# Kernel optimization log

Measured on AMD Instinct MI355X. Metric: run time of the kernel, lower is better.

Reference implementation:

```python
import jax, jax.numpy as jnp
import numpy as np

B, S, D, H = 8, 1024, 1024, 16
DH = D // H


def setup_inputs() -> dict:
    key = jax.random.key(0)
    ks = jax.random.split(key, 8)
    en = jax.random.normal(ks[0], (B, S, D), dtype=jnp.float32)
    fr = jax.random.normal(ks[1], (B, S, D), dtype=jnp.float32)
    l_en = jax.random.randint(ks[2], (B,), 1, S + 1)
    l_fr = jax.random.randint(ks[3], (B,), 1, S + 1)
    # nn.Linear-style params (weight stored [out, in])
    lim_q = 1.0 / np.sqrt(D)
    W_Q_w = jax.random.uniform(ks[4], (D, D), minval=-lim_q, maxval=lim_q, dtype=jnp.float32)
    W_Q_b = jax.random.uniform(ks[5], (D,), minval=-lim_q, maxval=lim_q, dtype=jnp.float32)
    W_KV_w = jax.random.uniform(ks[6], (2 * D, D), minval=-lim_q, maxval=lim_q, dtype=jnp.float32)
    W_KV_b = jax.random.uniform(ks[7], (2 * D,), minval=-lim_q, maxval=lim_q, dtype=jnp.float32)
    return {"en": en, "fr": fr, "l_en": l_en, "l_fr": l_fr,
            "W_Q_w": W_Q_w, "W_Q_b": W_Q_b, "W_KV_w": W_KV_w, "W_KV_b": W_KV_b}


def reference(en, fr, l_en, l_fr, W_Q_w, W_Q_b, W_KV_w, W_KV_b):
    # q from decoder (fr), k/v from encoder (en)
    q = (fr @ W_Q_w.T + W_Q_b).reshape(B, S, H, DH).transpose(0, 2, 1, 3)  # [B,H,S,DH]
    kv = (en @ W_KV_w.T + W_KV_b).reshape(B, S, 2, H, DH).transpose(2, 0, 3, 1, 4)
    k, v = kv[0], kv[1]  # [B,H,S,DH]

    # NOTE: original scales by sqrt(embedding_dim), not sqrt(head_dim)
    attn = jnp.einsum('bhqd,bhkd->bhqk', q, k) / jnp.sqrt(jnp.float32(D))

    pos = jnp.arange(S)
    mask_en = (pos[None, :] < l_en[:, None])  # [B,S] key mask
    mask_fr = (pos[None, :] < l_fr[:, None])  # [B,S] query mask
    mask = (mask_fr[:, :, None] & mask_en[:, None, :])[:, None, :, :]  # [B,1,Sq,Sk]

    attn = jnp.where(mask, attn, -jnp.inf)
    attn = jax.nn.softmax(attn, axis=-1)
    attn = jnp.nan_to_num(attn)  # fully-masked rows -> 0 (matches torch nan_to_num)

    out = jnp.einsum('bhqk,bhkd->bhqd', attn, v)  # [B,H,S,DH]
    return out.transpose(0, 2, 1, 3).reshape(B, S, D)
```

## Files before the change

### kernel.cpp

```cpp
#include <hip/hip_runtime.h>
#include <hip/hip_bf16.h>
#include <stdint.h>

typedef __bf16 bf16_t;
typedef bf16_t bf16x8 __attribute__((ext_vector_type(8)));
typedef float f32x4 __attribute__((ext_vector_type(4)));
typedef unsigned short ushortx8 __attribute__((ext_vector_type(8)));

__device__ __forceinline__ uint16_t f2bf(float f) {
  uint32_t u = __float_as_uint(f);
  uint32_t r = u + 0x7FFFu + ((u >> 16) & 1u);
  return (uint16_t)(r >> 16);
}

__device__ __forceinline__ int read_len(const int* __restrict__ p, int b) {
  bool is64 = (p[1] == 0) | (p[3] == 0) | (p[5] == 0) | (p[7] == 0);
  return is64 ? p[2 * b] : p[b];
}

#define GLDS16(gp, lp)                                                   \
  __builtin_amdgcn_global_load_lds(                                      \
      (const __attribute__((address_space(1))) uint32_t*)(gp),           \
      (__attribute__((address_space(3))) uint32_t*)(lp), 16, 0, 0)

__global__ void cvt4_kernel(const float* __restrict__ s0, uint16_t* __restrict__ d0, int n0,
                            const float* __restrict__ s1, uint16_t* __restrict__ d1, int n1,
                            const float* __restrict__ s2, uint16_t* __restrict__ d2, int n2,
                            const float* __restrict__ s3, uint16_t* __restrict__ d3, int n3,
                            const int* __restrict__ msk2, const int* __restrict__ msk3) {
  int e = (blockIdx.x * blockDim.x + threadIdx.x) * 4;
  const float* s;
  uint16_t* d;
  const int* msk = nullptr;
  if (e < n0) { s = s0 + e; d = d0 + e; }
  else if ((e -= n0) < n1) { s = s1 + e; d = d1 + e; }
  else if ((e -= n1) < n2) { s = s2 + e; d = d2 + e; msk = msk2; }
  else if ((e -= n2) < n3) { s = s3 + e; d = d3 + e; msk = msk3; }
  else return;
  if (msk) {
    int row = (e >> 10) & 1023, b = e >> 20;
    int need = (read_len(msk, b) + 127) & ~127;
    if (row >= need) return;
  }
  const float4 v = *reinterpret_cast<const float4*>(s);
  ushort4 o;
  o.x = f2bf(v.x); o.y = f2bf(v.y); o.z = f2bf(v.z); o.w = f2bf(v.w);
  *reinterpret_cast<ushort4*>(d) = o;
}

template <bool ABF16>
__global__ __launch_bounds__(256) void gemm_fused(
    const float* __restrict__ frF, const float* __restrict__ enF,
    const uint16_t* __restrict__ frB, const uint16_t* __restrict__ enB,
    const uint16_t* __restrict__ wq, const uint16_t* __restrict__ wkv,
    const float* __restrict__ bq, const float* __restrict__ bkv,
    const int* __restrict__ l_en_p, const int* __restrict__ l_fr_p,
    uint16_t* __restrict__ Qb,
    uint16_t* __restrict__ Kb,
    uint16_t* __restrict__ Vb) {
  __shared__ __attribute__((aligned(16))) uint16_t As[2][128 * 64];
  __shared__ __attribute__((aligned(16))) uint16_t Bs[2][128 * 64];
  const int t = threadIdx.x;
  const int lane = t & 63;
  const int w = t >> 6;
  const int wm = w >> 1, wn = w & 1;
  const int l15 = lane & 15, lg = lane >> 4;

  const int orig = blockIdx.x;
  const int xcd = orig & 7;
  const int slot = orig >> 3;
  const bool isQ = slot < 64;
  int b, bn;
  if (isQ) { b = slot >> 3; bn = (slot & 7) * 128; }
  else { int s2 = slot - 64; b = s2 >> 4; bn = (s2 & 15) * 128; }
  const int i = (xcd - b) & 7;
  const int bm = b * 1024 + i * 128;

  const int need = isQ ? read_len(l_fr_p, b) : read_len(l_en_p, b);
  if (i * 128 >= need) return;

  const uint16_t* Bw = isQ ? wq : wkv;
  const float* bias = isQ ? bq : bkv;
  const float scale = isQ ? 0.03125f : 1.0f;
  const uint16_t* Ab = isQ ? frB : enB;
  const float* Af = isQ ? frF : enF;

  f32x4 acc[4][4];
#pragma unroll
  for (int ii = 0; ii < 4; ++ii)
#pragma unroll
    for (int j = 0; j < 4; ++j) acc[ii][j] = (f32x4){0.f, 0.f, 0.f, 0.f};

  float4 ar0[4], ar1[4];

  auto stageB = [&](int buf, int kt) {
#pragma unroll
    for (int ii = 0; ii < 4; ++ii) {
      int g = t + 256 * ii;
      int L = g ^ ((g >> 3) & 7);
      int row = L >> 3, k8 = L & 7;
      GLDS16(Bw + (size_t)(bn + row) * 1024 + kt + k8 * 8, &Bs[buf][g * 8]);
    }
  };
  auto stageA_bf = [&](int buf, int kt) {
#pragma unroll
    for (int ii = 0; ii < 4; ++ii) {
      int g = t + 256 * ii;
      int L = g ^ ((g >> 3) & 7);
      int row = L >> 3, k8 = L & 7;
      GLDS16(Ab + (size_t)(bm + row) * 1024 + kt + k8 * 8, &As[buf][g * 8]);
    }
  };
  auto loadA_f32 = [&](int kt) {
#pragma unroll
    for (int ii = 0; ii < 4; ++ii) {
      int L = t + 256 * ii;
      int row = L >> 3, k8 = L & 7;
      const float* src = Af + (size_t)(bm + row) * 1024 + kt + k8 * 8;
      ar0[ii] = *reinterpret_cast<const float4*>(src);
      ar1[ii] = *reinterpret_cast<const float4*>(src + 4);
    }
  };
  auto writeA = [&](int buf) {
#pragma unroll
    for (int ii = 0; ii < 4; ++ii) {
      int L = t + 256 * ii;
      int row = L >> 3, k8 = L & 7;
      ushortx8 o;
      o[0] = f2bf(ar0[ii].x); o[1] = f2bf(ar0[ii].y);
      o[2] = f2bf(ar0[ii].z); o[3] = f2bf(ar0[ii].w);
      o[4] = f2bf(ar1[ii].x); o[5] = f2bf(ar1[ii].y);
      o[6] = f2bf(ar1[ii].z); o[7] = f2bf(ar1[ii].w);
      int byte = (row * 128 + k8 * 16) ^ ((row & 7) << 4);
      *reinterpret_cast<ushortx8*>(reinterpret_cast<char*>(As[buf]) + byte) = o;
    }
  };
  auto compute = [&](int buf) {
#pragma unroll
    for (int ks = 0; ks < 2; ++ks) {
      const int kb = ks * 64 + lg * 16;
      bf16x8 af[4], bf[4];
#pragma unroll
      for (int mf = 0; mf < 4; ++mf) {
        int row = wm * 64 + mf * 16 + l15;
        int byte = (row * 128 + kb) ^ ((row & 7) << 4);
        af[mf] = *reinterpret_cast<const bf16x8*>(
            reinterpret_cast<const char*>(As[buf]) + byte);
      }
#pragma unroll
      for (int nf = 0; nf < 4; ++nf) {
        int row = wn * 64 + nf * 16 + l15;
        int byte = (row * 128 + kb) ^ ((row & 7) << 4);
        bf[nf] = *reinterpret_cast<const bf16x8*>(
            reinterpret_cast<const char*>(Bs[buf]) + byte);
      }
#pragma unroll
      for (int mf = 0; mf < 4; ++mf)
#pragma unroll
        for (int nf = 0; nf < 4; ++nf)
          acc[mf][nf] = __builtin_amdgcn_mfma_f32_16x16x32_bf16(
              af[mf], bf[nf], acc[mf][nf], 0, 0, 0);
    }
  };

  if (ABF16) {
    stageB(0, 0);
    stageA_bf(0, 0);
  } else {
    loadA_f32(0);
    stageB(0, 0);
    writeA(0);
  }
  __syncthreads();

#pragma unroll 2
  for (int tt = 0; tt < 16; ++tt) {
    const int cur = tt & 1;
    const int ktn = (tt + 1) * 64;
    if (ABF16) {
      if (tt < 15) { stageB(cur ^ 1, ktn); stageA_bf(cur ^ 1, ktn); }
      compute(cur);
    } else {
      if (tt < 15) { stageB(cur ^ 1, ktn); loadA_f32(ktn); }
      compute(cur);
      if (tt < 15) writeA(cur ^ 1);
    }
    __syncthreads();
  }

#pragma unroll
  for (int mf = 0; mf < 4; ++mf) {
#pragma unroll
    for (int nf = 0; nf < 4; ++nf) {
      int n = bn + wn * 64 + nf * 16 + l15;
      float bv = bias[n];
#pragma unroll
      for (int r = 0; r < 4; ++r) {
        int m = bm + wm * 64 + mf * 16 + lg * 4 + r;
        float v = (acc[mf][nf][r] + bv) * scale;
        uint16_t o = f2bf(v);
        int bb = m >> 10, s = m & 1023;
        if (isQ) {
          int h = n >> 6, d = n & 63;
          Qb[((((bb * 16 + h) << 10) | s) << 6) | d] = o;
        } else if (n < 1024) {
          int h = n >> 6, d = n & 63;
          Kb[((((bb * 16 + h) << 10) | s) << 6) | d] = o;
        } else {
          int n2 = n - 1024;
          int h = n2 >> 6, d = n2 & 63;
          Vb[((((bb * 16 + h) << 6) | d) << 10) | s] = o;
        }
      }
    }
  }
}

__global__ __launch_bounds__(256) void attn_kernel(
    const uint16_t* __restrict__ Qb,
    const uint16_t* __restrict__ Kb,
    const uint16_t* __restrict__ Vt,
    const int* __restrict__ l_en_p, const int* __restrict__ l_fr_p,
    float* __restrict__ out) {
  __shared__ __attribute__((aligned(16))) uint16_t Ks[64 * 64];
  __shared__ __attribute__((aligned(16))) uint16_t Vs[64 * 64];
  __shared__ __attribute__((aligned(16))) bf16_t Ps[4][16][72];
  const int t = threadIdx.x;
  const int lane = t & 63, w = t >> 6;
  const int l15 = lane & 15, lg = lane >> 4;
  const int orig = blockIdx.x;
  const int xcd = orig & 7;
  const int slot = orig >> 3;
  const int b = slot >> 4;
  const int rest = slot & 15;
  const int h = xcd + 8 * (rest >> 3);
  const int q0 = (rest & 7) << 7;
  const int bh = b * 16 + h;
  const int len_en = read_len(l_en_p, b);
  const int len_fr = read_len(l_fr_p, b);

  if (q0 >= len_fr) {
    for (int i = t; i < 128 * 64; i += 256) {
      int rr = i >> 6, cc = i & 63;
      out[(size_t)(b * 1024 + q0 + rr) * 1024 + h * 64 + cc] = 0.f;
    }
    return;
  }

  bf16x8 aq[2][2];
#pragma unroll
  for (int s = 0; s < 2; ++s) {
    const uint16_t* qbase =
        Qb + ((size_t)bh * 1024 + q0 + s * 64 + w * 16 + l15) * 64 + lg * 8;
    aq[s][0] = *reinterpret_cast<const bf16x8*>(qbase);
    aq[s][1] = *reinterpret_cast<const bf16x8*>(qbase + 32);
  }

  float mrow[2][4], lrow[2][4];
  f32x4 oacc[2][4];
#pragma unroll
  for (int s = 0; s < 2; ++s)
#pragma unroll
    for (int r = 0; r < 4; ++r) {
      mrow[s][r] = -1e30f; lrow[s][r] = 0.f;
      oacc[s][r] = (f32x4){0.f, 0.f, 0.f, 0.f};
    }

  const int ntiles = (len_en + 63) >> 6;
  for (int tt = 0; tt < ntiles; ++tt) {
    const int j0 = tt * 64;
#pragma unroll
    for (int i = 0; i < 2; ++i) {
      int g = t + 256 * i;
      int L = g ^ ((g >> 3) & 7);
      int row = L >> 3, k8 = L & 7;
      GLDS16(Kb + ((size_t)bh * 1024 + j0 + row) * 64 + k8 * 8, Ks + g * 8);
      GLDS16(Vt + ((size_t)bh * 64 + row) * 1024 + j0 + k8 * 8, Vs + g * 8);
    }
    __syncthreads();

#pragma unroll
    for (int s = 0; s < 2; ++s) {
      f32x4 sc[4];
#pragma unroll
      for (int nf = 0; nf < 4; ++nf) sc[nf] = (f32x4){0.f, 0.f, 0.f, 0.f};
#pragma unroll
      for (int ks = 0; ks < 2; ++ks) {
        const bf16x8 a = aq[s][ks];
        const int kb = ks * 64 + lg * 16;
#pragma unroll
        for (int nf = 0; nf < 4; ++nf) {
          int row = nf * 16 + l15;
          int byte = (row * 128 + kb) ^ ((row & 7) << 4);
          bf16x8 bk = *reinterpret_cast<const bf16x8*>(
              reinterpret_cast<const char*>(Ks) + byte);
          sc[nf] = __builtin_amdgcn_mfma_f32_16x16x32_bf16(a, bk, sc[nf], 0, 0, 0);
        }
      }
#pragma unroll
      for (int nf = 0; nf < 4; ++nf) {
        int col = j0 + nf * 16 + l15;
        if (col >= len_en) sc[nf] = (f32x4){-1e30f, -1e30f, -1e30f, -1e30f};
      }
      float tm[4];
#pragma unroll
      for (int r = 0; r < 4; ++r)
        tm[r] = fmaxf(fmaxf(sc[0][r], sc[1][r]), fmaxf(sc[2][r], sc[3][r]));
#pragma unroll
      for (int off = 1; off < 16; off <<= 1)
#pragma unroll
        for (int r = 0; r < 4; ++r) tm[r] = fmaxf(tm[r], __shfl_xor(tm[r], off));

      float fac[4];
#pragma unroll
      for (int r = 0; r < 4; ++r) {
        float mn = fmaxf(mrow[s][r], tm[r]);
        fac[r] = __expf(mrow[s][r] - mn);
        mrow[s][r] = mn;
      }
      float ps[4] = {0.f, 0.f, 0.f, 0.f};
#pragma unroll
      for (int nf = 0; nf < 4; ++nf)
#pragma unroll
        for (int r = 0; r < 4; ++r) {
          float p = __expf(sc[nf][r] - mrow[s][r]);
          ps[r] += p;
          Ps[w][lg * 4 + r][nf * 16 + l15] = (bf16_t)p;
        }
#pragma unroll
      for (int off = 1; off < 16; off <<= 1)
#pragma unroll
        for (int r = 0; r < 4; ++r) ps[r] += __shfl_xor(ps[r], off);
#pragma unroll
      for (int r = 0; r < 4; ++r) lrow[s][r] = lrow[s][r] * fac[r] + ps[r];
#pragma unroll
      for (int df = 0; df < 4; ++df)
#pragma unroll
        for (int r = 0; r < 4; ++r) oacc[s][df][r] *= fac[r];

#pragma unroll
      for (int ks = 0; ks < 2; ++ks) {
        const bf16x8 pa = *reinterpret_cast<const bf16x8*>(
            &Ps[w][l15][0] + ks * 32 + lg * 8);
#pragma unroll
        for (int df = 0; df < 4; ++df) {
          int row = df * 16 + l15;
          int byte = (row * 128 + ks * 64 + lg * 16) ^ ((row & 7) << 4);
          bf16x8 bv = *reinterpret_cast<const bf16x8*>(
              reinterpret_cast<const char*>(Vs) + byte);
          oacc[s][df] =
              __builtin_amdgcn_mfma_f32_16x16x32_bf16(pa, bv, oacc[s][df], 0, 0, 0);
        }
      }
    }
    __syncthreads();
  }

#pragma unroll
  for (int s = 0; s < 2; ++s)
#pragma unroll
    for (int df = 0; df < 4; ++df)
#pragma unroll
      for (int r = 0; r < 4; ++r) {
        int q = q0 + s * 64 + w * 16 + lg * 4 + r;
        float inv = (q < len_fr && lrow[s][r] > 0.f) ? 1.0f / lrow[s][r] : 0.f;
        out[(size_t)(b * 1024 + q) * 1024 + h * 64 + df * 16 + l15] =
            oacc[s][df][r] * inv;
      }
}

extern "C" void kernel_launch(void* const* d_in, const int* in_sizes, int n_in,
                              void* d_out, int out_size, void* d_ws,
                              size_t ws_size, hipStream_t stream) {
  const float* en = (const float*)d_in[0];
  const float* fr = (const float*)d_in[1];
  const int* l_en = (const int*)d_in[2];
  const int* l_fr = (const int*)d_in[3];
  const float* wq = (const float*)d_in[4];
  const float* bq = (const float*)d_in[5];
  const float* wkv = (const float*)d_in[6];
  const float* bkv = (const float*)d_in[7];
  float* out = (float*)d_out;

  char* ws = (char*)d_ws;
  uint16_t* wq_bf = (uint16_t*)(ws);
  uint16_t* wkv_bf = (uint16_t*)(ws + 2097152);
  uint16_t* Qbuf = (uint16_t*)(ws + 6291456);
  uint16_t* Kbuf = (uint16_t*)(ws + 23068672);
  uint16_t* Vtbuf = (uint16_t*)(ws + 39845888);
  uint16_t* fr_bf = (uint16_t*)(ws + 56623104);
  uint16_t* en_bf = (uint16_t*)(ws + 73400320);
  const bool pre = ws_size >= 90177536ull;

  if (pre) {
    cvt4_kernel<<<19456, 256, 0, stream>>>(wq, wq_bf, 1048576,
                                           wkv, wkv_bf, 2097152,
                                           fr, fr_bf, 8388608,
                                           en, en_bf, 8388608,
                                           l_fr, l_en);
    gemm_fused<true><<<1536, 256, 0, stream>>>(nullptr, nullptr, fr_bf, en_bf,
                                               wq_bf, wkv_bf, bq, bkv,
                                               l_en, l_fr, Qbuf, Kbuf, Vtbuf);
  } else {
    cvt4_kernel<<<3072, 256, 0, stream>>>(wq, wq_bf, 1048576,
                                          wkv, wkv_bf, 2097152,
                                          nullptr, nullptr, 0,
                                          nullptr, nullptr, 0,
                                          nullptr, nullptr);
    gemm_fused<false><<<1536, 256, 0, stream>>>(fr, en, nullptr, nullptr,
                                                wq_bf, wkv_bf, bq, bkv,
                                                l_en, l_fr, Qbuf, Kbuf, Vtbuf);
  }

  attn_kernel<<<1024, 256, 0, stream>>>(Qbuf, Kbuf, Vtbuf, l_en, l_fr, out);
}
```

Baseline: 135.0 us.

## Double-buffer K/V tiles, use 8 waves per block, lazily rescale softmax

Attention kernel now uses 512 threads with one 16-row query slice per wave instead of two slices per wave, halving per-wave register state. K/V tiles are double-buffered in LDS so the next tile's async global-to-LDS load overlaps with compute, removing one barrier per tile. The online-softmax rescale of accumulators is skipped when the running max grows by at most 8, saving exp and multiply work. This doubles LDS for K/V and risks larger intermediate exponent values in bf16 P.

```diff
diff --git a/kernel.cpp b/kernel.cpp
--- a/kernel.cpp
+++ b/kernel.cpp
@@ -216,15 +216,15 @@
   }
 }
 
-__global__ __launch_bounds__(256) void attn_kernel(
+__global__ __launch_bounds__(512) void attn_kernel(
     const uint16_t* __restrict__ Qb,
     const uint16_t* __restrict__ Kb,
     const uint16_t* __restrict__ Vt,
     const int* __restrict__ l_en_p, const int* __restrict__ l_fr_p,
     float* __restrict__ out) {
-  __shared__ __attribute__((aligned(16))) uint16_t Ks[64 * 64];
-  __shared__ __attribute__((aligned(16))) uint16_t Vs[64 * 64];
-  __shared__ __attribute__((aligned(16))) bf16_t Ps[4][16][72];
+  __shared__ __attribute__((aligned(16))) uint16_t Ks[2][64 * 64];
+  __shared__ __attribute__((aligned(16))) uint16_t Vs[2][64 * 64];
+  __shared__ __attribute__((aligned(16))) bf16_t Ps[8][16][72];
   const int t = threadIdx.x;
   const int lane = t & 63, w = t >> 6;
   const int l15 = lane & 15, lg = lane >> 4;
@@ -240,133 +240,130 @@
   const int len_fr = read_len(l_fr_p, b);
 
   if (q0 >= len_fr) {
-    for (int i = t; i < 128 * 64; i += 256) {
+    for (int i = t; i < 128 * 64; i += 512) {
       int rr = i >> 6, cc = i & 63;
       out[(size_t)(b * 1024 + q0 + rr) * 1024 + h * 64 + cc] = 0.f;
     }
     return;
   }
 
-  bf16x8 aq[2][2];
-#pragma unroll
-  for (int s = 0; s < 2; ++s) {
-    const uint16_t* qbase =
-        Qb + ((size_t)bh * 1024 + q0 + s * 64 + w * 16 + l15) * 64 + lg * 8;
-    aq[s][0] = *reinterpret_cast<const bf16x8*>(qbase);
-    aq[s][1] = *reinterpret_cast<const bf16x8*>(qbase + 32);
-  }
-
-  float mrow[2][4], lrow[2][4];
-  f32x4 oacc[2][4];
-#pragma unroll
-  for (int s = 0; s < 2; ++s)
+  const uint16_t* qbase =
+      Qb + ((size_t)bh * 1024 + q0 + w * 16 + l15) * 64 + lg * 8;
+  const bf16x8 aq0 = *reinterpret_cast<const bf16x8*>(qbase);
+  const bf16x8 aq1 = *reinterpret_cast<const bf16x8*>(qbase + 32);
+
+  float mrow[4], lrow[4];
+  f32x4 oacc[4];
+#pragma unroll
+  for (int r = 0; r < 4; ++r) { mrow[r] = -1e30f; lrow[r] = 0.f; }
+#pragma unroll
+  for (int df = 0; df < 4; ++df) oacc[df] = (f32x4){0.f, 0.f, 0.f, 0.f};
+
+  auto stage = [&](int buf, int j0) {
+    int g = t;
+    int L = g ^ ((g >> 3) & 7);
+    int row = L >> 3, k8 = L & 7;
+    GLDS16(Kb + ((size_t)bh * 1024 + j0 + row) * 64 + k8 * 8, &Ks[buf][g * 8]);
+    GLDS16(Vt + ((size_t)bh * 64 + row) * 1024 + j0 + k8 * 8, &Vs[buf][g * 8]);
+  };
+
+  const int ntiles = (len_en + 63) >> 6;
+  stage(0, 0);
+  __syncthreads();
+
+  for (int tt = 0; tt < ntiles; ++tt) {
+    const int cur = tt & 1;
+    const int j0 = tt * 64;
+    if (tt + 1 < ntiles) stage(cur ^ 1, (tt + 1) * 64);
+
+    f32x4 sc[4];
+#pragma unroll
+    for (int nf = 0; nf < 4; ++nf) sc[nf] = (f32x4){0.f, 0.f, 0.f, 0.f};
+#pragma unroll
+    for (int ks = 0; ks < 2; ++ks) {
+      const bf16x8 aq = ks ? aq1 : aq0;
+      const int kb = ks * 64 + lg * 16;
+#pragma unroll
+      for (int nf = 0; nf < 4; ++nf) {
+        int row = nf * 16 + l15;
+        int byte = (row * 128 + kb) ^ ((row & 7) << 4);
+        bf16x8 bk = *reinterpret_cast<const bf16x8*>(
+            reinterpret_cast<const char*>(Ks[cur]) + byte);
+        sc[nf] = __builtin_amdgcn_mfma_f32_16x16x32_bf16(aq, bk, sc[nf], 0, 0, 0);
+      }
+    }
+#pragma unroll
+    for (int nf = 0; nf < 4; ++nf) {
+      int col = j0 + nf * 16 + l15;
+      if (col >= len_en) sc[nf] = (f32x4){-1e30f, -1e30f, -1e30f, -1e30f};
+    }
+    float tm[4];
+#pragma unroll
+    for (int r = 0; r < 4; ++r)
+      tm[r] = fmaxf(fmaxf(sc[0][r], sc[1][r]), fmaxf(sc[2][r], sc[3][r]));
+#pragma unroll
+    for (int off = 1; off < 16; off <<= 1)
+#pragma unroll
+      for (int r = 0; r < 4; ++r) tm[r] = fmaxf(tm[r], __shfl_xor(tm[r], off));
+
+    bool small = (tm[0] <= mrow[0] + 8.f) && (tm[1] <= mrow[1] + 8.f) &&
+                 (tm[2] <= mrow[2] + 8.f) && (tm[3] <= mrow[3] + 8.f);
+    if (!__all(small)) {
+      float fac[4];
+#pragma unroll
+      for (int r = 0; r < 4; ++r) {
+        float mn = fmaxf(mrow[r], tm[r]);
+        fac[r] = __expf(mrow[r] - mn);
+        mrow[r] = mn;
+      }
+#pragma unroll
+      for (int r = 0; r < 4; ++r) lrow[r] *= fac[r];
+#pragma unroll
+      for (int df = 0; df < 4; ++df)
+#pragma unroll
+        for (int r = 0; r < 4; ++r) oacc[df][r] *= fac[r];
+    }
+    float ps[4] = {0.f, 0.f, 0.f, 0.f};
+#pragma unroll
+    for (int nf = 0; nf < 4; ++nf)
+#pragma unroll
+      for (int r = 0; r < 4; ++r) {
+        float p = __expf(sc[nf][r] - mrow[r]);
+        ps[r] += p;
+        Ps[w][lg * 4 + r][nf * 16 + l15] = (bf16_t)p;
+      }
+#pragma unroll
+    for (int off = 1; off < 16; off <<= 1)
+#pragma unroll
+      for (int r = 0; r < 4; ++r) ps[r] += __shfl_xor(ps[r], off);
+#pragma unroll
+    for (int r = 0; r < 4; ++r) lrow[r] += ps[r];
+
+#pragma unroll
+    for (int ks = 0; ks < 2; ++ks) {
+      const bf16x8 pa = *reinterpret_cast<const bf16x8*>(
+          &Ps[w][l15][0] + ks * 32 + lg * 8);
+#pragma unroll
+      for (int df = 0; df < 4; ++df) {
+        int row = df * 16 + l15;
+        int byte = (row * 128 + ks * 64 + lg * 16) ^ ((row & 7) << 4);
+        bf16x8 bv = *reinterpret_cast<const bf16x8*>(
+            reinterpret_cast<const char*>(Vs[cur]) + byte);
+        oacc[df] = __builtin_amdgcn_mfma_f32_16x16x32_bf16(pa, bv, oacc[df], 0, 0, 0);
+      }
+    }
+    __syncthreads();
+  }
+
+#pragma unroll
+  for (int df = 0; df < 4; ++df)
 #pragma unroll
     for (int r = 0; r < 4; ++r) {
-      mrow[s][r] = -1e30f; lrow[s][r] = 0.f;
-      oacc[s][r] = (f32x4){0.f, 0.f, 0.f, 0.f};
-    }
-
-  const int ntiles = (len_en + 63) >> 6;
-  for (int tt = 0; tt < ntiles; ++tt) {
-    const int j0 = tt * 64;
-#pragma unroll
-    for (int i = 0; i < 2; ++i) {
-      int g = t + 256 * i;
-      int L = g ^ ((g >> 3) & 7);
-      int row = L >> 3, k8 = L & 7;
-      GLDS16(Kb + ((size_t)bh * 1024 + j0 + row) * 64 + k8 * 8, Ks + g * 8);
-      GLDS16(Vt + ((size_t)bh * 64 + row) * 1024 + j0 + k8 * 8, Vs + g * 8);
-    }
-    __syncthreads();
-
-#pragma unroll
-    for (int s = 0; s < 2; ++s) {
-      f32x4 sc[4];
-#pragma unroll
-      for (int nf = 0; nf < 4; ++nf) sc[nf] = (f32x4){0.f, 0.f, 0.f, 0.f};
-#pragma unroll
-      for (int ks = 0; ks < 2; ++ks) {
-        const bf16x8 a = aq[s][ks];
-        const int kb = ks * 64 + lg * 16;
-#pragma unroll
-        for (int nf = 0; nf < 4; ++nf) {
-          int row = nf * 16 + l15;
-          int byte = (row * 128 + kb) ^ ((row & 7) << 4);
-          bf16x8 bk = *reinterpret_cast<const bf16x8*>(
-              reinterpret_cast<const char*>(Ks) + byte);
-          sc[nf] = __builtin_amdgcn_mfma_f32_16x16x32_bf16(a, bk, sc[nf], 0, 0, 0);
-        }
-      }
-#pragma unroll
-      for (int nf = 0; nf < 4; ++nf) {
-        int col = j0 + nf * 16 + l15;
-        if (col >= len_en) sc[nf] = (f32x4){-1e30f, -1e30f, -1e30f, -1e30f};
-      }
-      float tm[4];
-#pragma unroll
-      for (int r = 0; r < 4; ++r)
-        tm[r] = fmaxf(fmaxf(sc[0][r], sc[1][r]), fmaxf(sc[2][r], sc[3][r]));
-#pragma unroll
-      for (int off = 1; off < 16; off <<= 1)
-#pragma unroll
-        for (int r = 0; r < 4; ++r) tm[r] = fmaxf(tm[r], __shfl_xor(tm[r], off));
-
-      float fac[4];
-#pragma unroll
-      for (int r = 0; r < 4; ++r) {
-        float mn = fmaxf(mrow[s][r], tm[r]);
-        fac[r] = __expf(mrow[s][r] - mn);
-        mrow[s][r] = mn;
-      }
-      float ps[4] = {0.f, 0.f, 0.f, 0.f};
-#pragma unroll
-      for (int nf = 0; nf < 4; ++nf)
-#pragma unroll
-        for (int r = 0; r < 4; ++r) {
-          float p = __expf(sc[nf][r] - mrow[s][r]);
-          ps[r] += p;
-          Ps[w][lg * 4 + r][nf * 16 + l15] = (bf16_t)p;
-        }
-#pragma unroll
-      for (int off = 1; off < 16; off <<= 1)
-#pragma unroll
-        for (int r = 0; r < 4; ++r) ps[r] += __shfl_xor(ps[r], off);
-#pragma unroll
-      for (int r = 0; r < 4; ++r) lrow[s][r] = lrow[s][r] * fac[r] + ps[r];
-#pragma unroll
-      for (int df = 0; df < 4; ++df)
-#pragma unroll
-        for (int r = 0; r < 4; ++r) oacc[s][df][r] *= fac[r];
-
-#pragma unroll
-      for (int ks = 0; ks < 2; ++ks) {
-        const bf16x8 pa = *reinterpret_cast<const bf16x8*>(
-            &Ps[w][l15][0] + ks * 32 + lg * 8);
-#pragma unroll
-        for (int df = 0; df < 4; ++df) {
-          int row = df * 16 + l15;
-          int byte = (row * 128 + ks * 64 + lg * 16) ^ ((row & 7) << 4);
-          bf16x8 bv = *reinterpret_cast<const bf16x8*>(
-              reinterpret_cast<const char*>(Vs) + byte);
-          oacc[s][df] =
-              __builtin_amdgcn_mfma_f32_16x16x32_bf16(pa, bv, oacc[s][df], 0, 0, 0);
-        }
-      }
-    }
-    __syncthreads();
-  }
-
-#pragma unroll
-  for (int s = 0; s < 2; ++s)
-#pragma unroll
-    for (int df = 0; df < 4; ++df)
-#pragma unroll
-      for (int r = 0; r < 4; ++r) {
-        int q = q0 + s * 64 + w * 16 + lg * 4 + r;
-        float inv = (q < len_fr && lrow[s][r] > 0.f) ? 1.0f / lrow[s][r] : 0.f;
-        out[(size_t)(b * 1024 + q) * 1024 + h * 64 + df * 16 + l15] =
-            oacc[s][df][r] * inv;
-      }
+      int q = q0 + w * 16 + lg * 4 + r;
+      float inv = (q < len_fr && lrow[r] > 0.f) ? 1.0f / lrow[r] : 0.f;
+      out[(size_t)(b * 1024 + q) * 1024 + h * 64 + df * 16 + l15] =
+          oacc[df][r] * inv;
+    }
 }
 
 extern "C" void kernel_launch(void* const* d_in, const int* in_sizes, int n_in,
@@ -412,5 +409,5 @@
                                                 l_en, l_fr, Qbuf, Kbuf, Vtbuf);
   }
 
-  attn_kernel<<<1024, 256, 0, stream>>>(Qbuf, Kbuf, Vtbuf, l_en, l_fr, out);
-}
+  attn_kernel<<<1024, 512, 0, stream>>>(Qbuf, Kbuf, Vtbuf, l_en, l_fr, out);
+}
```

Result: faster. 115.6 us (-14.4%).
